# Kernel tuning notes

Hardware: AMD Instinct MI355X
Metric: run time of the kernel (lower is better)

## Reference

```python
import jax, jax.numpy as jnp
import numpy as np

B, H, W, IN_C = 2, 64, 64, 3
D = 192            # embed_dim
DEPTH = 4
DI = 2 * D         # d_inner (mamba expand=2)
DS = 16            # d_state
DC = 4             # d_conv
DTR = -(-D // 16)  # dt_rank = ceil(D/16) = 12
EPS = 1e-5


def setup_inputs() -> dict:
    key = jax.random.key(0)
    ks = jax.random.split(key, 8)
    def rn(k, shape, s=0.02):
        return jax.random.normal(k, shape, dtype=jnp.float32) * s
    x = jax.random.normal(ks[0], (B, IN_C, H, W), dtype=jnp.float32)
    proj_w = rn(ks[1], (D, IN_C))
    proj_b = jnp.zeros((D,), jnp.float32)
    lp_w = rn(ks[2], (DEPTH, D, 2 * D))          # linear_proj: (out=D, in=2D)
    lp_b = jnp.zeros((DEPTH, D), jnp.float32)
    norm_w = jnp.ones((DEPTH, D), jnp.float32)
    in_w = rn(ks[3], (DEPTH, 2 * DI, D))         # mamba in_proj (no bias)
    conv_w = rn(ks[4], (DEPTH, DI, DC), 0.1)     # depthwise causal conv1d
    conv_b = jnp.zeros((DEPTH, DI), jnp.float32)
    xproj_w = rn(ks[5], (DEPTH, DTR + 2 * DS, DI))
    dt_w = rn(ks[6], (DEPTH, DI, DTR), 0.1)
    dt0 = np.random.default_rng(0).uniform(1e-3, 0.1, size=(DEPTH, DI)).astype(np.float32)
    dt_b = jnp.asarray(np.log(np.expm1(dt0)))    # softplus-inverse init (mamba default)
    A_log = jnp.tile(jnp.log(jnp.arange(1, DS + 1, dtype=jnp.float32)), (DEPTH, DI, 1))
    Dp = jnp.ones((DEPTH, DI), jnp.float32)
    out_w = rn(ks[7], (DEPTH, D, DI))
    normf_w = jnp.ones((D,), jnp.float32)
    return dict(x=x, proj_w=proj_w, proj_b=proj_b, lp_w=lp_w, lp_b=lp_b,
                norm_w=norm_w, in_w=in_w, conv_w=conv_w, conv_b=conv_b,
                xproj_w=xproj_w, dt_w=dt_w, dt_b=dt_b, A_log=A_log, Dp=Dp,
                out_w=out_w, normf_w=normf_w)


def _rmsnorm(x, w):
    return x * jax.lax.rsqrt(jnp.mean(x * x, axis=-1, keepdims=True) + EPS) * w


def _mamba(x, in_w, conv_w, conv_b, xproj_w, dt_w, dt_b, A_log, Dp, out_w):
    # x: (B, N, D)
    Bsz = x.shape[0]
    xz = jnp.einsum('bnd,ed->bne', x, in_w)                 # (B,N,2*DI)
    xi, z = jnp.split(xz, 2, axis=-1)
    # causal depthwise conv1d along sequence (pad left d_conv-1)
    xt = xi.transpose(0, 2, 1)                              # (B,DI,N)
    xc = jax.lax.conv_general_dilated(xt, conv_w[:, None, :], (1,), [(DC - 1, 0)],
                                      feature_group_count=DI)
    xi = jax.nn.silu((xc + conv_b[None, :, None]).transpose(0, 2, 1))  # (B,N,DI)
    dbc = jnp.einsum('bni,ei->bne', xi, xproj_w)            # (B,N,DTR+2*DS)
    dt = jax.nn.softplus(jnp.einsum('bnr,ir->bni', dbc[..., :DTR], dt_w) + dt_b)
    Bm = dbc[..., DTR:DTR + DS]                             # (B,N,DS)
    Cm = dbc[..., DTR + DS:]                                # (B,N,DS)
    A = -jnp.exp(A_log)                                     # (DI,DS)
    dA = jnp.exp(dt[..., None] * A)                         # (B,N,DI,DS)
    dBx = dt[..., None] * Bm[:, :, None, :] * xi[..., None] # (B,N,DI,DS)
    def step(h, inp):
        a, bx = inp
        h = a * h + bx
        return h, h
    h0 = jnp.zeros((Bsz, DI, DS), x.dtype)
    _, hs = jax.lax.scan(step, h0, (dA.transpose(1, 0, 2, 3), dBx.transpose(1, 0, 2, 3)))
    y = jnp.einsum('nbis,bns->bni', hs, Cm) + Dp * xi
    y = y * jax.nn.silu(z)
    return jnp.einsum('bni,di->bnd', y, out_w)


def _block(x, lp_w, lp_b, norm_w, mp):
    # DeltaVisionMambaBlock: token-diff -> linear_proj -> RMSNorm -> Mamba -> +skip
    prev = jnp.concatenate([jnp.zeros_like(x[:, :1]), x[:, :-1]], axis=1)
    comb = jnp.concatenate([x, x - prev], axis=-1)          # (B,N,2D)
    proj = jnp.einsum('bnc,dc->bnd', comb, lp_w) + lp_b
    return _mamba(_rmsnorm(proj, norm_w), *mp) + x


def reference(x, proj_w, proj_b, lp_w, lp_b, norm_w, in_w, conv_w, conv_b,
              xproj_w, dt_w, dt_b, A_log, Dp, out_w, normf_w):
    Bsz = x.shape[0]
    feat = jnp.einsum('bchw,dc->bdhw', x, proj_w) + proj_b[None, :, None, None]
    seq = feat.reshape(Bsz, D, H * W).transpose(0, 2, 1)    # (B,N,D)
    for l in range(DEPTH):
        mp = (in_w[l], conv_w[l], conv_b[l], xproj_w[l], dt_w[l], dt_b[l],
              A_log[l], Dp[l], out_w[l])
        seq = _block(seq, lp_w[l], lp_b[l], norm_w[l], mp)
    seq = _rmsnorm(seq, normf_w)
    return seq.transpose(0, 2, 1).reshape(Bsz, D, H, W)
```

## Files before the change

kernel.cpp:

```cpp
#include <hip/hip_runtime.h>
#include <hip/hip_bf16.h>

#define BB 2
#define NN 4096
#define DD 192
#define DI 384
#define DS 16
#define DTR 12
#define DC 4
#define DEPTH 4
#define NT (BB*NN)
#define NCH 256
#define CL 16
#define EPSF 1e-5f

#define OFF_X       0
#define OFF_PROJ_W  24576
#define OFF_PROJ_B  25152
#define OFF_LP_W    25344
#define OFF_LP_B    320256
#define OFF_NORM_W  321024
#define OFF_IN_W    321792
#define OFF_CONV_W  911616
#define OFF_CONV_B  917760
#define OFF_XPROJ_W 919296
#define OFF_DT_W    986880
#define OFF_DT_B    1005312
#define OFF_A_LOG   1006848
#define OFF_DP      1031424
#define OFF_OUT_W   1032960
#define OFF_NORMF_W 1327872
#define ARENA_TOTAL 1328064
#define ARENA_BYTES 2656160

typedef __hip_bfloat16 bf16_t;
typedef unsigned short u16;
typedef unsigned int u32;
typedef __attribute__((ext_vector_type(8))) unsigned short u16x8;
typedef __attribute__((ext_vector_type(8))) short s16x8;
typedef __attribute__((ext_vector_type(4))) float f32x4;

struct Ptrs { const void* p[16]; };

__device__ __forceinline__ float bf(u16 v){ return __uint_as_float(((u32)v)<<16); }
__device__ __forceinline__ u16 f2bf(float f){
  u32 b = __float_as_uint(f);
  return (u16)((b + 0x7FFFu + ((b>>16)&1u)) >> 16);
}

__global__ __launch_bounds__(256) void k_detect(const u16* __restrict__ x, int* flag){
  __shared__ int cnt;
  if (threadIdx.x==0) cnt=0;
  __syncthreads();
  u32 v = x[2*threadIdx.x];
  int ex = (int)((v>>7)&0xFF);
  if (ex>=100 && ex<=140) atomicAdd(&cnt,1);
  __syncthreads();
  if (threadIdx.x==0) *flag = (cnt>128) ? 0 : 1;
}

__global__ __launch_bounds__(256) void k_cvt(Ptrs ps, const int* __restrict__ flag, u16* __restrict__ arena){
  int e = blockIdx.x*256 + threadIdx.x;
  if (e >= ARENA_TOTAL) return;
  const void* sp; int off;
  if      (e < OFF_PROJ_W ){ sp=ps.p[0];  off=OFF_X; }
  else if (e < OFF_PROJ_B ){ sp=ps.p[1];  off=OFF_PROJ_W; }
  else if (e < OFF_LP_W   ){ sp=ps.p[2];  off=OFF_PROJ_B; }
  else if (e < OFF_LP_B   ){ sp=ps.p[3];  off=OFF_LP_W; }
  else if (e < OFF_NORM_W ){ sp=ps.p[4];  off=OFF_LP_B; }
  else if (e < OFF_IN_W   ){ sp=ps.p[5];  off=OFF_NORM_W; }
  else if (e < OFF_CONV_W ){ sp=ps.p[6];  off=OFF_IN_W; }
  else if (e < OFF_CONV_B ){ sp=ps.p[7];  off=OFF_CONV_W; }
  else if (e < OFF_XPROJ_W){ sp=ps.p[8];  off=OFF_CONV_B; }
  else if (e < OFF_DT_W   ){ sp=ps.p[9];  off=OFF_XPROJ_W; }
  else if (e < OFF_DT_B   ){ sp=ps.p[10]; off=OFF_DT_W; }
  else if (e < OFF_A_LOG  ){ sp=ps.p[11]; off=OFF_DT_B; }
  else if (e < OFF_DP     ){ sp=ps.p[12]; off=OFF_A_LOG; }
  else if (e < OFF_OUT_W  ){ sp=ps.p[13]; off=OFF_DP; }
  else if (e < OFF_NORMF_W){ sp=ps.p[14]; off=OFF_OUT_W; }
  else                     { sp=ps.p[15]; off=OFF_NORMF_W; }
  int k = e - off;
  if (*flag){
    u32 v = ((const u32*)sp)[k];
    arena[e] = (u16)((v + 0x7FFFu + ((v>>16)&1u)) >> 16);
  } else {
    arena[e] = ((const u16*)sp)[k];
  }
}

__global__ __launch_bounds__(256) void k_proj(const u16* __restrict__ x, const u16* __restrict__ pw,
                                              const u16* __restrict__ pb, float* __restrict__ seq){
  int idx = blockIdx.x*256 + threadIdx.x;
  if (idx >= NT*DD) return;
  int d = idx % DD; int bn = idx / DD; int b = bn >> 12; int n = bn & (NN-1);
  float acc = bf(pb[d]);
  acc += bf(x[(b*3+0)*NN + n]) * bf(pw[d*3+0]);
  acc += bf(x[(b*3+1)*NN + n]) * bf(pw[d*3+1]);
  acc += bf(x[(b*3+2)*NN + n]) * bf(pw[d*3+2]);
  seq[idx] = acc;
}

__global__ __launch_bounds__(256) void k_lp_norm(const float* __restrict__ seq,
    const u16* __restrict__ lp_w, const u16* __restrict__ lp_b, const u16* __restrict__ norm_w,
    u16* __restrict__ xn){
  const int tid = threadIdx.x;
  const int n0 = blockIdx.x*16;
  __shared__ u16 combL[16][392];
  __shared__ u16 wL[192][72];
  __shared__ float accL[16][200];
  __shared__ float ssq[16];
  const int w = tid>>6, lane = tid&63, lm = lane&15, lk = lane>>4;

  for (int idx = tid*4; idx < 16*DD; idx += 1024){
    int t = idx/DD, d = idx%DD;
    int gn = n0 + t;
    float4 cur = *(const float4*)&seq[gn*DD + d];
    float4 prv = make_float4(0.f,0.f,0.f,0.f);
    if ((gn & (NN-1)) != 0) prv = *(const float4*)&seq[(gn-1)*DD + d];
    combL[t][d+0]=f2bf(cur.x); combL[t][d+1]=f2bf(cur.y); combL[t][d+2]=f2bf(cur.z); combL[t][d+3]=f2bf(cur.w);
    combL[t][DD+d+0]=f2bf(cur.x-prv.x); combL[t][DD+d+1]=f2bf(cur.y-prv.y);
    combL[t][DD+d+2]=f2bf(cur.z-prv.z); combL[t][DD+d+3]=f2bf(cur.w-prv.w);
  }
  f32x4 acc[3];
  #pragma unroll
  for (int i=0;i<3;++i) acc[i] = (f32x4){0.f,0.f,0.f,0.f};
  for (int c=0;c<6;++c){
    for (int idx = tid*8; idx < 192*64; idx += 2048){
      int row = idx >> 6, col = idx & 63;
      *(u16x8*)&wL[row][col] = *(const u16x8*)(lp_w + row*384 + c*64 + col);
    }
    __syncthreads();
    #pragma unroll
    for (int ks=0; ks<2; ++ks){
      s16x8 a = *(s16x8*)&combL[lm][c*64 + ks*32 + lk*8];
      #pragma unroll
      for (int nt=0; nt<3; ++nt){
        s16x8 b = *(s16x8*)&wL[(w*3+nt)*16 + lm][ks*32 + lk*8];
        acc[nt] = __builtin_amdgcn_mfma_f32_16x16x32_bf16(a, b, acc[nt], 0, 0, 0);
      }
    }
    __syncthreads();
  }
  #pragma unroll
  for (int nt=0; nt<3; ++nt)
    #pragma unroll
    for (int r=0; r<4; ++r){
      int m = lk*4 + r;
      int n = (w*3+nt)*16 + lm;
      accL[m][n] = acc[nt][r] + bf(lp_b[n]);
    }
  __syncthreads();
  {
    int tok = tid >> 4, j = tid & 15;
    float s = 0.f;
    #pragma unroll
    for (int c2=0;c2<12;++c2){ float v = accL[tok][j*12+c2]; s += v*v; }
    s += __shfl_xor(s,1); s += __shfl_xor(s,2); s += __shfl_xor(s,4); s += __shfl_xor(s,8);
    if (j==0) ssq[tok] = rsqrtf(s*(1.f/DD) + EPSF);
  }
  __syncthreads();
  for (int idx = tid; idx < 16*DD; idx += 256){
    int t = idx/DD, d = idx%DD;
    xn[(n0+t)*DD + d] = f2bf(accL[t][d] * ssq[t] * bf(norm_w[d]));
  }
}

__global__ __launch_bounds__(256) void k_inproj(const u16* __restrict__ xn,
    const u16* __restrict__ in_w, u16* __restrict__ xi_c, u16* __restrict__ zz_b){
  const int tid = threadIdx.x;
  const int m0 = blockIdx.x*64;
  const int e0 = blockIdx.y*64;
  __shared__ u16 aL[64][200];
  __shared__ u16 bL[64][200];
  for (int idx = tid*8; idx < 64*192; idx += 2048){
    int row = idx/192, col = idx%192;
    *(u16x8*)&aL[row][col] = *(const u16x8*)(xn   + (m0+row)*192 + col);
    *(u16x8*)&bL[row][col] = *(const u16x8*)(in_w + (e0+row)*192 + col);
  }
  __syncthreads();
  const int w = tid >> 6, lane = tid & 63;
  const int lm = lane & 15, lk = lane >> 4;
  f32x4 acc[4];
  #pragma unroll
  for (int i=0;i<4;++i) acc[i] = (f32x4){0.f,0.f,0.f,0.f};
  #pragma unroll
  for (int ks=0; ks<6; ++ks){
    s16x8 a = *(s16x8*)&aL[w*16 + lm][ks*32 + lk*8];
    #pragma unroll
    for (int nt=0; nt<4; ++nt){
      s16x8 b = *(s16x8*)&bL[nt*16 + lm][ks*32 + lk*8];
      acc[nt] = __builtin_amdgcn_mfma_f32_16x16x32_bf16(a, b, acc[nt], 0, 0, 0);
    }
  }
  #pragma unroll
  for (int nt=0; nt<4; ++nt){
    int e = e0 + nt*16 + lm;
    #pragma unroll
    for (int r=0; r<4; ++r){
      int tok = m0 + w*16 + lk*4 + r;
      u16 v = f2bf(acc[nt][r]);
      if (e0 < DI) xi_c[tok*DI + e]      = v;
      else         zz_b[tok*DI + e - DI] = v;
    }
  }
}

__global__ __launch_bounds__(256) void k_xds(const u16* __restrict__ xi_c,
    const u16* __restrict__ conv_w, const u16* __restrict__ conv_b,
    const u16* __restrict__ xproj_w, const u16* __restrict__ dt_w, const u16* __restrict__ dt_bv,
    const u16* __restrict__ A_log,
    u16* __restrict__ xc_g, float* __restrict__ dt_g, float* __restrict__ Bm, float* __restrict__ Cm,
    float* __restrict__ P, float* __restrict__ Q){
  const int tid = threadIdx.x;
  const int n0 = blockIdx.x*16;
  const int basei = n0 & ~(NN-1);
  const int b = n0 >> 12;
  const int ch = (n0 & (NN-1)) >> 4;
  __shared__ u16 xcL[16][392];
  __shared__ float dtL[16][388];
  __shared__ u16 dtwL[384][24];
  __shared__ float dbcL[16][16];
  __shared__ float bmL[16][16];
  ((float*)dbcL)[tid] = 0.f;
  for (int idx=tid*8; idx<16*384; idx+=2048){
    int r=idx/384, c=idx%384;
    int gn = n0 + r;
    float vals[4][8];
    #pragma unroll
    for (int q=0;q<4;++q){
      int row = gn-3+q;
      if (row >= basei){
        u16x8 xv = *(const u16x8*)(xi_c + row*DI + c);
        #pragma unroll
        for (int j=0;j<8;++j) vals[q][j] = bf(xv[j]);
      } else {
        #pragma unroll
        for (int j=0;j<8;++j) vals[q][j] = 0.f;
      }
    }
    u16x8 cw0 = *(const u16x8*)(conv_w + c*4);
    u16x8 cw1 = *(const u16x8*)(conv_w + c*4 + 8);
    u16x8 cw2 = *(const u16x8*)(conv_w + c*4 + 16);
    u16x8 cw3 = *(const u16x8*)(conv_w + c*4 + 24);
    u16x8 cb  = *(const u16x8*)(conv_b + c);
    u16x8 ov;
    #pragma unroll
    for (int j=0;j<8;++j){
      u16 cwa, cwb, cwc, cwd;
      int jj = j*4;
      if (jj < 8)       { cwa=cw0[jj];    cwb=cw0[jj+1];  cwc=cw0[jj+2];  cwd=cw0[jj+3]; }
      else if (jj < 16) { cwa=cw1[jj-8];  cwb=cw1[jj-7];  cwc=cw1[jj-6];  cwd=cw1[jj-5]; }
      else if (jj < 24) { cwa=cw2[jj-16]; cwb=cw2[jj-15]; cwc=cw2[jj-14]; cwd=cw2[jj-13]; }
      else              { cwa=cw3[jj-24]; cwb=cw3[jj-23]; cwc=cw3[jj-22]; cwd=cw3[jj-21]; }
      float acc = bf(cb[j]) + vals[0][j]*bf(cwa) + vals[1][j]*bf(cwb) + vals[2][j]*bf(cwc) + vals[3][j]*bf(cwd);
      float v = acc/(1.f+__expf(-acc));
      ov[j] = f2bf(v);
    }
    *(u16x8*)&xcL[r][c] = ov;
    *(u16x8*)(xc_g + gn*DI + c) = ov;
  }
  for (int idx=tid; idx<384*12; idx+=256){
    int r2=idx/12, c2=idx%12;
    dtwL[r2][c2] = dt_w[idx];
    dtwL[r2][12+c2] = 0;
  }
  __syncthreads();
  const int w = tid>>6, lane = tid&63, lm = lane&15, lk = lane>>4;
  const s16x8 zb = {0,0,0,0,0,0,0,0};
  if (w < 3){
    f32x4 acc = {0.f,0.f,0.f,0.f};
    #pragma unroll
    for (int ks=0; ks<12; ++ks){
      s16x8 a = *(s16x8*)&xcL[lm][ks*32 + lk*8];
      s16x8 bb = (w < 2 || lm < 12) ? *(const s16x8*)(xproj_w + (w*16+lm)*384 + ks*32 + lk*8) : zb;
      acc = __builtin_amdgcn_mfma_f32_16x16x32_bf16(a, bb, acc, 0, 0, 0);
    }
    int e = w*16 + lm;
    #pragma unroll
    for (int r=0;r<4;++r){
      int m = lk*4 + r;
      int gm = n0 + m;
      if      (e < 12) dbcL[m][e] = acc[r];
      else if (e < 28){ Bm[gm*DS + e-12] = acc[r]; bmL[m][e-12] = acc[r]; }
      else if (e < 44) Cm[gm*DS + e-28] = acc[r];
    }
  }
  __syncthreads();
  s16x8 a_dt = zb;
  if (lk < 2){
    #pragma unroll
    for (int j=0;j<8;++j) a_dt[j] = (short)f2bf(dbcL[lm][lk*8+j]);
  }
  #pragma unroll
  for (int q=0;q<6;++q){
    int nt = w*6 + q;
    s16x8 bb = (lk<2) ? *(s16x8*)&dtwL[nt*16+lm][lk*8] : zb;
    f32x4 acc = {0.f,0.f,0.f,0.f};
    acc = __builtin_amdgcn_mfma_f32_16x16x32_bf16(a_dt, bb, acc, 0, 0, 0);
    int i = nt*16 + lm;
    float bias = bf(dt_bv[i]);
    #pragma unroll
    for (int r=0;r<4;++r){
      int m = lk*4 + r;
      float xval = acc[r] + bias;
      float sp = (xval>20.f)? xval : log1pf(__expf(xval));
      dtL[m][i] = sp;
      dt_g[(n0+m)*DI + i] = sp;
    }
  }
  __syncthreads();
  for (int cc=0; cc<2; ++cc){
    int i = tid + cc*256;
    if (i >= DI) break;
    float Av[DS];
    {
      u16x8 a0 = *(const u16x8*)(A_log + i*DS);
      u16x8 a1 = *(const u16x8*)(A_log + i*DS + 8);
      #pragma unroll
      for (int s=0;s<8;++s){ Av[s] = -__expf(bf(a0[s])); Av[8+s] = -__expf(bf(a1[s])); }
    }
    float Pv[DS], h[DS];
    #pragma unroll
    for (int s=0;s<DS;++s){ Pv[s]=1.f; h[s]=0.f; }
    #pragma unroll 4
    for (int t=0;t<CL;++t){
      float dtv = dtL[t][i];
      float xv  = bf(xcL[t][i]);
      float dtx = dtv*xv;
      #pragma unroll
      for (int s=0;s<DS;++s){
        float a = __expf(dtv*Av[s]);
        Pv[s] *= a;
        h[s] = a*h[s] + dtx*bmL[t][s];
      }
    }
    const int base = ((b*DI + i)*NCH + ch)*DS;
    #pragma unroll
    for (int s4=0;s4<4;++s4){
      *(float4*)&P[base+s4*4] = make_float4(Pv[s4*4+0],Pv[s4*4+1],Pv[s4*4+2],Pv[s4*4+3]);
      *(float4*)&Q[base+s4*4] = make_float4(h[s4*4+0],h[s4*4+1],h[s4*4+2],h[s4*4+3]);
    }
  }
}

__global__ __launch_bounds__(256) void k_scan2(const float* __restrict__ P, const float* __restrict__ Q,
                                               float* __restrict__ Hin){
  int tid = blockIdx.x*256 + threadIdx.x;
  int s = tid & 15; int ci = tid >> 4;
  float h = 0.f;
  for (int ch=0; ch<NCH; ++ch){
    int idx = (ci*NCH+ch)*DS + s;
    Hin[idx] = h;
    h = P[idx]*h + Q[idx];
  }
}

__global__ __launch_bounds__(128) void k_scan3(const float* __restrict__ dt,
    const u16* __restrict__ xc, const float* __restrict__ Bm, const float* __restrict__ Cm,
    const u16* __restrict__ zz_b, const u16* __restrict__ A_log, const u16* __restrict__ Dp,
    const float* __restrict__ Hin, u16* __restrict__ Y){
  const int tid = threadIdx.x;
  const int i = blockIdx.x*128 + tid;
  const int ch = blockIdx.y, b = blockIdx.z;
  __shared__ float bm_l[CL][DS], cm_l[CL][DS];
  {
    int r = (tid>>2)&15, c4 = (tid&3)*4;
    if (tid < 64)       *(float4*)&bm_l[r][c4] = *(const float4*)&Bm[(b*NN + ch*CL + r)*DS + c4];
    else                *(float4*)&cm_l[r][c4] = *(const float4*)&Cm[(b*NN + ch*CL + r)*DS + c4];
  }
  float Av[DS];
  {
    u16x8 a0 = *(const u16x8*)(A_log + i*DS);
    u16x8 a1 = *(const u16x8*)(A_log + i*DS + 8);
    #pragma unroll
    for (int s=0;s<8;++s){ Av[s] = -__expf(bf(a0[s])); Av[8+s] = -__expf(bf(a1[s])); }
  }
  const float Dv = bf(Dp[i]);
  float h[DS];
  const int base = ((b*DI + i)*NCH + ch)*DS;
  #pragma unroll
  for (int s4=0;s4<4;++s4){
    float4 hv = *(const float4*)&Hin[base+s4*4];
    h[s4*4+0]=hv.x; h[s4*4+1]=hv.y; h[s4*4+2]=hv.z; h[s4*4+3]=hv.w;
  }
  __syncthreads();
  const int nb = b*NN + ch*CL;
  #pragma unroll 4
  for (int t=0;t<CL;++t){
    float xv  = bf(xc[(nb+t)*DI + i]);
    float dtv = dt[(nb+t)*DI + i];
    float zv  = bf(zz_b[(nb+t)*DI + i]);
    float dtx = dtv*xv;
    float y = 0.f;
    #pragma unroll
    for (int s=0;s<DS;++s){
      float a = __expf(dtv*Av[s]);
      h[s] = a*h[s] + dtx*bm_l[t][s];
      y += h[s]*cm_l[t][s];
    }
    y += Dv*xv;
    y *= zv/(1.f+__expf(-zv));
    Y[(nb+t)*DI + i] = f2bf(y);
  }
}

__global__ __launch_bounds__(256) void k_out(const u16* __restrict__ Y,
    const u16* __restrict__ out_w, float* __restrict__ seq){
  const int tid = threadIdx.x;
  const int m0 = blockIdx.x*64;
  const int d0 = blockIdx.y*64;
  __shared__ u16 aL[64][200];
  __shared__ u16 bL[64][200];
  const int w = tid >> 6, lane = tid & 63;
  const int lm = lane & 15, lk = lane >> 4;
  f32x4 acc[4];
  #pragma unroll
  for (int i=0;i<4;++i) acc[i] = (f32x4){0.f,0.f,0.f,0.f};
  for (int c=0; c<2; ++c){
    const int kc = c*192;
    for (int idx = tid*8; idx < 64*192; idx += 2048){
      int row = idx/192, col = idx%192;
      *(u16x8*)&aL[row][col] = *(const u16x8*)(Y     + (m0+row)*DI + kc + col);
      *(u16x8*)&bL[row][col] = *(const u16x8*)(out_w + (d0+row)*DI + kc + col);
    }
    __syncthreads();
    #pragma unroll
    for (int ks=0; ks<6; ++ks){
      s16x8 a = *(s16x8*)&aL[w*16 + lm][ks*32 + lk*8];
      #pragma unroll
      for (int nt=0; nt<4; ++nt){
        s16x8 b = *(s16x8*)&bL[nt*16 + lm][ks*32 + lk*8];
        acc[nt] = __builtin_amdgcn_mfma_f32_16x16x32_bf16(a, b, acc[nt], 0, 0, 0);
      }
    }
    __syncthreads();
  }
  #pragma unroll
  for (int nt=0; nt<4; ++nt){
    int d = d0 + nt*16 + lm;
    #pragma unroll
    for (int r=0; r<4; ++r){
      int tok = m0 + w*16 + lk*4 + r;
      seq[tok*DD + d] += acc[nt][r];
    }
  }
}

__global__ __launch_bounds__(192) void k_final(const float* __restrict__ seq,
    const u16* __restrict__ normf_w, void* __restrict__ out, const int* __restrict__ flag){
  const int d = threadIdx.x;
  const int bn = blockIdx.x;
  const int b = bn >> 12, n = bn & (NN-1);
  __shared__ float wred[3];
  float v = seq[bn*DD + d];
  float s = v*v;
  #pragma unroll
  for (int off=32; off>=1; off>>=1) s += __shfl_down(s,off);
  if ((d&63)==0) wred[d>>6]=s;
  __syncthreads();
  float r = rsqrtf((wred[0]+wred[1]+wred[2])*(1.f/DD) + EPSF);
  float res = v * r * bf(normf_w[d]);
  int o = (b*DD+d)*NN + n;
  if (*flag) ((float*)out)[o] = res;
  else       ((u16*)out)[o]   = f2bf(res);
}

extern "C" void kernel_launch(void* const* d_in, const int* in_sizes, int n_in,
                              void* d_out, int out_size, void* d_ws, size_t ws_size,
                              hipStream_t stream){
  Ptrs ps;
  for (int i=0;i<16;++i) ps.p[i] = d_in[i];

  u16* arena = (u16*)d_ws;
  int* flag  = (int*)((char*)d_ws + ARENA_TOTAL*2);
  float* fbase = (float*)((char*)d_ws + ARENA_BYTES);

  float* seq  = fbase;
  float* dt   = seq  + NT*DD;
  float* Bm   = dt   + NT*DI;
  float* Cm   = Bm   + NT*DS;
  float* Hin  = Cm   + NT*DS;
  float* Pb   = Hin  + BB*DI*NCH*DS;
  float* Qb   = Pb   + BB*DI*NCH*DS;
  u16* xn_b   = (u16*)(Qb + BB*DI*NCH*DS);
  u16* xi_c   = xn_b + NT*DD;
  u16* zz_b   = xi_c + NT*DI;
  u16* Y_b    = zz_b + NT*DI;
  u16* xc_b   = Y_b  + NT*DI;

  const u16* xA      = arena + OFF_X;
  const u16* proj_w  = arena + OFF_PROJ_W;
  const u16* proj_b  = arena + OFF_PROJ_B;
  const u16* lp_w    = arena + OFF_LP_W;
  const u16* lp_b    = arena + OFF_LP_B;
  const u16* norm_w  = arena + OFF_NORM_W;
  const u16* in_w    = arena + OFF_IN_W;
  const u16* conv_w  = arena + OFF_CONV_W;
  const u16* conv_b  = arena + OFF_CONV_B;
  const u16* xproj_w = arena + OFF_XPROJ_W;
  const u16* dt_w    = arena + OFF_DT_W;
  const u16* dt_b    = arena + OFF_DT_B;
  const u16* A_log   = arena + OFF_A_LOG;
  const u16* Dp      = arena + OFF_DP;
  const u16* out_w   = arena + OFF_OUT_W;
  const u16* normf_w = arena + OFF_NORMF_W;

  k_detect<<<1, 256, 0, stream>>>((const u16*)d_in[0], flag);
  k_cvt<<<(ARENA_TOTAL+255)/256, 256, 0, stream>>>(ps, flag, arena);

  k_proj<<<(NT*DD+255)/256, 256, 0, stream>>>(xA, proj_w, proj_b, seq);
  for (int l=0; l<DEPTH; ++l){
    k_lp_norm<<<NT/16, 256, 0, stream>>>(seq, lp_w + l*DD*2*DD, lp_b + l*DD, norm_w + l*DD, xn_b);
    k_inproj<<<dim3(NT/64, 12), 256, 0, stream>>>(xn_b, in_w + l*2*DI*DD, xi_c, zz_b);
    k_xds<<<NT/16, 256, 0, stream>>>(xi_c, conv_w + l*DI*DC, conv_b + l*DI,
        xproj_w + l*(DTR+2*DS)*DI, dt_w + l*DI*DTR, dt_b + l*DI, A_log + l*DI*DS,
        xc_b, dt, Bm, Cm, Pb, Qb);
    k_scan2<<<(BB*DI*DS)/256, 256, 0, stream>>>(Pb, Qb, Hin);
    k_scan3<<<dim3(DI/128, NCH, BB), 128, 0, stream>>>(dt, xc_b, Bm, Cm, zz_b,
        A_log + l*DI*DS, Dp + l*DI, Hin, Y_b);
    k_out<<<dim3(NT/64, 3), 256, 0, stream>>>(Y_b, out_w + l*DD*DI, seq);
  }
  k_final<<<NT, 192, 0, stream>>>(seq, normf_w, d_out, flag);
}
```

Baseline: 557.7 us.

## Store dt as bf16, reorder P/Q/Hin layout, load dt_w directly

Stores the softplus dt intermediate as bf16 instead of fp32, halving its write and read traffic between the chunk kernel and the final scan. Reorders the P/Q/Hin chunk-state arrays to (batch, chunk, channel, state) so each chunk's writes and reads are contiguous across channels. Removes the shared-memory staging of dt_w and loads the B operand for the dt MFMA straight from global memory. The bf16 dt adds rounding error to the scan input.

```diff
diff --git a/kernel.cpp b/kernel.cpp
--- a/kernel.cpp
+++ b/kernel.cpp
@@ -37,6 +37,7 @@
 typedef unsigned short u16;
 typedef unsigned int u32;
 typedef __attribute__((ext_vector_type(8))) unsigned short u16x8;
+typedef __attribute__((ext_vector_type(4))) unsigned short u16x4;
 typedef __attribute__((ext_vector_type(8))) short s16x8;
 typedef __attribute__((ext_vector_type(4))) float f32x4;
 
@@ -209,7 +210,7 @@
     const u16* __restrict__ conv_w, const u16* __restrict__ conv_b,
     const u16* __restrict__ xproj_w, const u16* __restrict__ dt_w, const u16* __restrict__ dt_bv,
     const u16* __restrict__ A_log,
-    u16* __restrict__ xc_g, float* __restrict__ dt_g, float* __restrict__ Bm, float* __restrict__ Cm,
+    u16* __restrict__ xc_g, u16* __restrict__ dt_g, float* __restrict__ Bm, float* __restrict__ Cm,
     float* __restrict__ P, float* __restrict__ Q){
   const int tid = threadIdx.x;
   const int n0 = blockIdx.x*16;
@@ -218,7 +219,6 @@
   const int ch = (n0 & (NN-1)) >> 4;
   __shared__ u16 xcL[16][392];
   __shared__ float dtL[16][388];
-  __shared__ u16 dtwL[384][24];
   __shared__ float dbcL[16][16];
   __shared__ float bmL[16][16];
   ((float*)dbcL)[tid] = 0.f;
@@ -259,11 +259,6 @@
     *(u16x8*)&xcL[r][c] = ov;
     *(u16x8*)(xc_g + gn*DI + c) = ov;
   }
-  for (int idx=tid; idx<384*12; idx+=256){
-    int r2=idx/12, c2=idx%12;
-    dtwL[r2][c2] = dt_w[idx];
-    dtwL[r2][12+c2] = 0;
-  }
   __syncthreads();
   const int w = tid>>6, lane = tid&63, lm = lane&15, lk = lane>>4;
   const s16x8 zb = {0,0,0,0,0,0,0,0};
@@ -294,7 +289,18 @@
   #pragma unroll
   for (int q=0;q<6;++q){
     int nt = w*6 + q;
-    s16x8 bb = (lk<2) ? *(s16x8*)&dtwL[nt*16+lm][lk*8] : zb;
+    int row = nt*16 + lm;
+    s16x8 bb = zb;
+    if (lk == 0){
+      u16x4 p0 = *(const u16x4*)(dt_w + row*12);
+      u16x4 p1 = *(const u16x4*)(dt_w + row*12 + 4);
+      #pragma unroll
+      for (int j=0;j<4;++j){ bb[j] = (short)p0[j]; bb[4+j] = (short)p1[j]; }
+    } else if (lk == 1){
+      u16x4 p = *(const u16x4*)(dt_w + row*12 + 8);
+      #pragma unroll
+      for (int j=0;j<4;++j) bb[j] = (short)p[j];
+    }
     f32x4 acc = {0.f,0.f,0.f,0.f};
     acc = __builtin_amdgcn_mfma_f32_16x16x32_bf16(a_dt, bb, acc, 0, 0, 0);
     int i = nt*16 + lm;
@@ -305,7 +311,7 @@
       float xval = acc[r] + bias;
       float sp = (xval>20.f)? xval : log1pf(__expf(xval));
       dtL[m][i] = sp;
-      dt_g[(n0+m)*DI + i] = sp;
+      dt_g[(n0+m)*DI + i] = f2bf(sp);
     }
   }
   __syncthreads();
@@ -334,7 +340,7 @@
         h[s] = a*h[s] + dtx*bmL[t][s];
       }
     }
-    const int base = ((b*DI + i)*NCH + ch)*DS;
+    const int base = ((b*NCH + ch)*DI + i)*DS;
     #pragma unroll
     for (int s4=0;s4<4;++s4){
       *(float4*)&P[base+s4*4] = make_float4(Pv[s4*4+0],Pv[s4*4+1],Pv[s4*4+2],Pv[s4*4+3]);
@@ -346,16 +352,17 @@
 __global__ __launch_bounds__(256) void k_scan2(const float* __restrict__ P, const float* __restrict__ Q,
                                                float* __restrict__ Hin){
   int tid = blockIdx.x*256 + threadIdx.x;
-  int s = tid & 15; int ci = tid >> 4;
+  int s = tid & 15; int gi = tid >> 4;
+  int b = gi / DI, i = gi % DI;
   float h = 0.f;
   for (int ch=0; ch<NCH; ++ch){
-    int idx = (ci*NCH+ch)*DS + s;
+    int idx = ((b*NCH + ch)*DI + i)*DS + s;
     Hin[idx] = h;
     h = P[idx]*h + Q[idx];
   }
 }
 
-__global__ __launch_bounds__(128) void k_scan3(const float* __restrict__ dt,
+__global__ __launch_bounds__(128) void k_scan3(const u16* __restrict__ dt,
     const u16* __restrict__ xc, const float* __restrict__ Bm, const float* __restrict__ Cm,
     const u16* __restrict__ zz_b, const u16* __restrict__ A_log, const u16* __restrict__ Dp,
     const float* __restrict__ Hin, u16* __restrict__ Y){
@@ -377,7 +384,7 @@
   }
   const float Dv = bf(Dp[i]);
   float h[DS];
-  const int base = ((b*DI + i)*NCH + ch)*DS;
+  const int base = ((b*NCH + ch)*DI + i)*DS;
   #pragma unroll
   for (int s4=0;s4<4;++s4){
     float4 hv = *(const float4*)&Hin[base+s4*4];
@@ -388,7 +395,7 @@
   #pragma unroll 4
   for (int t=0;t<CL;++t){
     float xv  = bf(xc[(nb+t)*DI + i]);
-    float dtv = dt[(nb+t)*DI + i];
+    float dtv = bf(dt[(nb+t)*DI + i]);
     float zv  = bf(zz_b[(nb+t)*DI + i]);
     float dtx = dtv*xv;
     float y = 0.f;
@@ -476,8 +483,7 @@
   float* fbase = (float*)((char*)d_ws + ARENA_BYTES);
 
   float* seq  = fbase;
-  float* dt   = seq  + NT*DD;
-  float* Bm   = dt   + NT*DI;
+  float* Bm   = seq  + NT*DD;
   float* Cm   = Bm   + NT*DS;
   float* Hin  = Cm   + NT*DS;
   float* Pb   = Hin  + BB*DI*NCH*DS;
@@ -487,6 +493,7 @@
   u16* zz_b   = xi_c + NT*DI;
   u16* Y_b    = zz_b + NT*DI;
   u16* xc_b   = Y_b  + NT*DI;
+  u16* dt_b16 = xc_b + NT*DI;
 
   const u16* xA      = arena + OFF_X;
   const u16* proj_w  = arena + OFF_PROJ_W;
@@ -514,9 +521,9 @@
     k_inproj<<<dim3(NT/64, 12), 256, 0, stream>>>(xn_b, in_w + l*2*DI*DD, xi_c, zz_b);
     k_xds<<<NT/16, 256, 0, stream>>>(xi_c, conv_w + l*DI*DC, conv_b + l*DI,
         xproj_w + l*(DTR+2*DS)*DI, dt_w + l*DI*DTR, dt_b + l*DI, A_log + l*DI*DS,
-        xc_b, dt, Bm, Cm, Pb, Qb);
+        xc_b, dt_b16, Bm, Cm, Pb, Qb);
     k_scan2<<<(BB*DI*DS)/256, 256, 0, stream>>>(Pb, Qb, Hin);
-    k_scan3<<<dim3(DI/128, NCH, BB), 128, 0, stream>>>(dt, xc_b, Bm, Cm, zz_b,
+    k_scan3<<<dim3(DI/128, NCH, BB), 128, 0, stream>>>(dt_b16, xc_b, Bm, Cm, zz_b,
         A_log + l*DI*DS, Dp + l*DI, Hin, Y_b);
     k_out<<<dim3(NT/64, 3), 256, 0, stream>>>(Y_b, out_w + l*DD*DI, seq);
   }
```

Measured after the change: 525.0 us. 5.9% less time.
